# Kernel optimization log

Measured on AMD Instinct MI355X. Metric: run time of the kernel, lower is better.

The kernel has to match this reference:

```python
import jax, jax.numpy as jnp
import numpy as np

B, S, D = 4, 2048, 1024
E, H, K = 8, 2048, 2


def setup_inputs() -> dict:
    key = jax.random.key(0)
    k_x, k_g, k1, k2, k3 = jax.random.split(key, 5)
    x = jax.random.normal(k_x, (B, S, D), dtype=jnp.float32)
    # nn.Linear weight layout is [out, in]
    Wg = jax.random.normal(k_g, (E, D), dtype=jnp.float32) * 0.02   # gate
    W1 = jax.random.normal(k1, (E, H, D), dtype=jnp.float32) * 0.02  # fc1, stacked over experts
    W2 = jax.random.normal(k2, (E, H, D), dtype=jnp.float32) * 0.02  # fc2
    W3 = jax.random.normal(k3, (E, D, H), dtype=jnp.float32) * 0.02  # fc3
    return {"x": x, "Wg": Wg, "W1": W1, "W2": W2, "W3": W3}


def reference(x, Wg, W1, W2, W3):
    # gating
    scores = jnp.einsum("bsd,ed->bse", x, Wg)                 # [B,S,E]
    topk_scores, topk_idx = jax.lax.top_k(scores, K)          # [B,S,K]
    topk_probs = jax.nn.softmax(topk_scores, axis=-1)         # [B,S,K]
    # scatter top-k probs back to a dense [B,S,E] gate (indices are distinct per token)
    gating = jnp.sum(jax.nn.one_hot(topk_idx, E, dtype=x.dtype) * topk_probs[..., None], axis=-2)  # [B,S,E]
    # dense compute-all-experts SwiGLU (faithful to source)
    h1 = jnp.einsum("bsd,ehd->bseh", x, W1)                   # [B,S,E,H]
    h2 = jnp.einsum("bsd,ehd->bseh", x, W2)
    hidden = jax.nn.silu(h1) * h2
    expert_out = jnp.einsum("bseh,edh->bsed", hidden, W3)     # [B,S,E,D]
    y = jnp.einsum("bse,bsed->bsd", gating, expert_out)       # weighted combine
    return y
```

## Files before the change

kernel.cpp:

```cpp
#include <hip/hip_runtime.h>
#include <hip/hip_bf16.h>
#include <cstdint>
#include <cstddef>

typedef unsigned short u16;
typedef uint32_t u32;
typedef __attribute__((ext_vector_type(4))) float f32x4;
typedef __attribute__((ext_vector_type(8))) short bf16x8;

#define NTOK 8192
#define DIM  1024
#define HID  2048
#define NEXP 8
#define MAXT1 72
#define MAXT2 136

#define GLD16(g, l) __builtin_amdgcn_global_load_lds( \
    (const __attribute__((address_space(1))) void*)(g), \
    (__attribute__((address_space(3))) void*)(l), 16, 0, 0)

#define WAITV(n) asm volatile("s_waitcnt vmcnt(" #n ")" ::: "memory")

__device__ __forceinline__ u16 f2bf(float f) {
  __hip_bfloat16 h = __float2bfloat16(f);
  return __builtin_bit_cast(u16, h);
}
__device__ __forceinline__ float bf2f(short s) {
  u32 u = ((u32)(u16)s) << 16;
  return __builtin_bit_cast(float, u);
}

__device__ __forceinline__ const bf16x8* lds_frag(const u16* base, int row, int chunk) {
  return (const bf16x8*)(base + row * 64 + ((chunk ^ (row & 7)) << 3));
}

__global__ __launch_bounds__(256) void convert_bf16_kernel(
    const float4* __restrict__ src, ushort4* __restrict__ dst, int n4) {
  int stride = gridDim.x * blockDim.x;
  for (int i = blockIdx.x * blockDim.x + threadIdx.x; i < n4; i += stride) {
    float4 v = src[i];
    ushort4 o;
    o.x = f2bf(v.x); o.y = f2bf(v.y); o.z = f2bf(v.z); o.w = f2bf(v.w);
    dst[i] = o;
  }
}

__global__ __launch_bounds__(256) void gating_kernel(
    const float4* __restrict__ x4, const float4* __restrict__ Wg4,
    int* __restrict__ gate_idx, float* __restrict__ gate_prob,
    u16* __restrict__ Xb) {
  int tid = threadIdx.x, w = tid >> 6, l = tid & 63;
  int t = blockIdx.x * 4 + w;

  float4 xv[4];
#pragma unroll
  for (int j = 0; j < 4; ++j)
    xv[j] = x4[(size_t)t * 256 + l + 64 * j];

  float acc[NEXP];
#pragma unroll
  for (int e = 0; e < NEXP; ++e) acc[e] = 0.f;
#pragma unroll
  for (int e = 0; e < NEXP; ++e)
#pragma unroll
    for (int j = 0; j < 4; ++j) {
      float4 wv = Wg4[e * 256 + l + 64 * j];
      acc[e] += xv[j].x * wv.x + xv[j].y * wv.y + xv[j].z * wv.z + xv[j].w * wv.w;
    }

#pragma unroll
  for (int j = 0; j < 4; ++j) {
    ushort4 o;
    o.x = f2bf(xv[j].x); o.y = f2bf(xv[j].y);
    o.z = f2bf(xv[j].z); o.w = f2bf(xv[j].w);
    *(ushort4*)&Xb[(size_t)t * DIM + (l + 64 * j) * 4] = o;
  }

#pragma unroll
  for (int off = 32; off >= 1; off >>= 1)
#pragma unroll
    for (int e = 0; e < NEXP; ++e)
      acc[e] += __shfl_xor(acc[e], off);

  if (l == 0) {
    float best = -1e30f, sec = -1e30f;
    int bi = 0, si = 0;
#pragma unroll
    for (int e = 0; e < NEXP; ++e) {
      float s = acc[e];
      if (s > best)      { sec = best; si = bi; best = s; bi = e; }
      else if (s > sec)  { sec = s; si = e; }
    }
    float e1  = __expf(sec - best);
    float inv = 1.f / (1.f + e1);
    gate_idx[t * 2]      = bi;
    gate_idx[t * 2 + 1]  = si;
    gate_prob[t * 2]     = inv;
    gate_prob[t * 2 + 1] = e1 * inv;
  }
}

__global__ __launch_bounds__(256) void hist_kernel(
    const int* __restrict__ gate_idx, int* __restrict__ counts) {
  __shared__ int h[NEXP];
  int tid = threadIdx.x;
  if (tid < NEXP) h[tid] = 0;
  __syncthreads();
  int i = blockIdx.x * 256 + tid;
  atomicAdd(&h[gate_idx[i]], 1);
  __syncthreads();
  if (tid < NEXP) atomicAdd(&counts[tid], h[tid]);
}

__global__ void scan_kernel(const int* __restrict__ counts,
                            int* __restrict__ offs, int* __restrict__ cursors,
                            int* __restrict__ tileE1, int* __restrict__ tileRow1,
                            int* __restrict__ nt1,
                            int* __restrict__ tileE2, int* __restrict__ tileRow2,
                            int* __restrict__ nt2) {
  if (threadIdx.x == 0 && blockIdx.x == 0) {
    int s = 0;
    for (int e = 0; e < NEXP; ++e) { offs[e] = s; cursors[e] = s; s += counts[e]; }
    int n1 = 0, n2 = 0;
    for (int e = 0; e < NEXP; ++e) {
      for (int r = 0; r < counts[e]; r += 256) { tileE1[n1] = e; tileRow1[n1] = r; ++n1; }
      for (int r = 0; r < counts[e]; r += 128) { tileE2[n2] = e; tileRow2[n2] = r; ++n2; }
    }
    *nt1 = n1; *nt2 = n2;
  }
}

__global__ __launch_bounds__(256) void scatter_kernel(
    const int* __restrict__ gate_idx, int* __restrict__ cursors,
    int* __restrict__ list, int* __restrict__ pos_of) {
  __shared__ int lc[NEXP];
  __shared__ int lbase[NEXP];
  int tid = threadIdx.x;
  if (tid < NEXP) lc[tid] = 0;
  __syncthreads();
  int i = blockIdx.x * 256 + tid;
  int e = gate_idx[i];
  int lp = atomicAdd(&lc[e], 1);
  __syncthreads();
  if (tid < NEXP) lbase[tid] = atomicAdd(&cursors[tid], lc[tid]);
  __syncthreads();
  int pos = lbase[e] + lp;
  list[pos] = i;
  pos_of[i] = pos;
}

__global__ __launch_bounds__(512, 2) void gemm1_kernel(
    const u16* __restrict__ Xb, const u16* __restrict__ W1b,
    const u16* __restrict__ W2b, const int* __restrict__ list,
    const int* __restrict__ offs, const int* __restrict__ counts,
    const int* __restrict__ tileE, const int* __restrict__ tileRow,
    const int* __restrict__ n_tiles, u16* __restrict__ hidden) {
  int flat = blockIdx.x + MAXT1 * blockIdx.y;
  int nf = (flat & 7) * (MAXT1 * (HID / 128) / 8) + (flat >> 3);
  int bx = nf % MAXT1;
  int tn = nf / MAXT1;
  if (bx >= *n_tiles) return;
  int e = tileE[bx], row0 = tileRow[bx];
  int n_e = counts[e], off_e = offs[e];
  __shared__ u16 As[2][256 * 64];
  __shared__ u16 B1s[2][128 * 64];
  __shared__ u16 B2s[2][128 * 64];
  int tid = threadIdx.x, w = tid >> 6, l = tid & 63;
  const u16* W1e = W1b + (size_t)e * HID * DIM;
  const u16* W2e = W2b + (size_t)e * HID * DIM;

  int schunk = ((l & 7) ^ (l >> 3)) * 8;
  u32 offA[4];
#pragma unroll
  for (int j = 0; j < 4; ++j) {
    int r = w * 32 + j * 8 + (l >> 3);
    int idx = row0 + r;
    int entry = list[off_e + (idx < n_e ? idx : 0)];
    offA[j] = (u32)(entry >> 1) * DIM + schunk;
  }
  u32 offB[2];
#pragma unroll
  for (int j = 0; j < 2; ++j) {
    int r = w * 16 + j * 8 + (l >> 3);
    offB[j] = (u32)(tn * 128 + r) * DIM + schunk;
  }

#define STAGE1(buf, kt) do { u32 kof_ = (u32)(kt) * 64;                        \
    _Pragma("unroll")                                                          \
    for (int j = 0; j < 4; ++j) GLD16(Xb + offA[j] + kof_, &As[buf][w * 2048 + j * 512]); \
    _Pragma("unroll")                                                          \
    for (int j = 0; j < 2; ++j) {                                              \
      GLD16(W1e + offB[j] + kof_, &B1s[buf][w * 1024 + j * 512]);              \
      GLD16(W2e + offB[j] + kof_, &B2s[buf][w * 1024 + j * 512]);              \
    } } while (0)

  f32x4 acc1[4][4], acc2[4][4];
#pragma unroll
  for (int mi = 0; mi < 4; ++mi)
#pragma unroll
    for (int ni = 0; ni < 4; ++ni) {
      acc1[mi][ni] = (f32x4){0.f, 0.f, 0.f, 0.f};
      acc2[mi][ni] = (f32x4){0.f, 0.f, 0.f, 0.f};
    }
  int wm = w >> 1, wn = w & 1;

  STAGE1(0, 0);
  STAGE1(1, 1);
  for (int kt = 0; kt < DIM / 64; ++kt) {
    if (kt < DIM / 64 - 1) { WAITV(8); } else { WAITV(0); }
    __builtin_amdgcn_s_barrier();
    int cur = kt & 1;
    const u16* Ab  = As[cur];
    const u16* B1b = B1s[cur];
    const u16* B2b = B2s[cur];
#pragma unroll
    for (int ks = 0; ks < 2; ++ks) {
      bf16x8 a[4], b1[4], b2[4];
#pragma unroll
      for (int mi = 0; mi < 4; ++mi)
        a[mi] = *lds_frag(Ab, wm * 64 + mi * 16 + (l & 15), ks * 4 + (l >> 4));
#pragma unroll
      for (int ni = 0; ni < 4; ++ni) {
        b1[ni] = *lds_frag(B1b, wn * 64 + ni * 16 + (l & 15), ks * 4 + (l >> 4));
        b2[ni] = *lds_frag(B2b, wn * 64 + ni * 16 + (l & 15), ks * 4 + (l >> 4));
      }
#pragma unroll
      for (int mi = 0; mi < 4; ++mi)
#pragma unroll
        for (int ni = 0; ni < 4; ++ni) {
          acc1[mi][ni] = __builtin_amdgcn_mfma_f32_16x16x32_bf16(a[mi], b1[ni], acc1[mi][ni], 0, 0, 0);
          acc2[mi][ni] = __builtin_amdgcn_mfma_f32_16x16x32_bf16(a[mi], b2[ni], acc2[mi][ni], 0, 0, 0);
        }
    }
    asm volatile("" ::: "memory");
    __builtin_amdgcn_s_barrier();
    if (kt + 2 < DIM / 64) STAGE1(cur, kt + 2);
  }

#pragma unroll
  for (int mi = 0; mi < 4; ++mi) {
#pragma unroll
    for (int i = 0; i < 4; ++i) {
      int m_loc = wm * 64 + mi * 16 + (l >> 4) * 4 + i;
      int idx = row0 + m_loc;
      if (idx < n_e) {
        size_t pos = (size_t)(off_e + idx);
#pragma unroll
        for (int ni = 0; ni < 4; ++ni) {
          int h_loc = tn * 128 + wn * 64 + ni * 16 + (l & 15);
          float h1 = acc1[mi][ni][i];
          float h2 = acc2[mi][ni][i];
          float hv = h1 / (1.f + __expf(-h1)) * h2;
          hidden[pos * HID + h_loc] = f2bf(hv);
        }
      }
    }
  }
}

__global__ __launch_bounds__(256, 2) void gemm2_kernel(
    const u16* __restrict__ hidden, const u16* __restrict__ W3b,
    const int* __restrict__ offs, const int* __restrict__ counts,
    const int* __restrict__ tileE, const int* __restrict__ tileRow,
    const int* __restrict__ n_tiles, u16* __restrict__ eout) {
  int flat = blockIdx.x + MAXT2 * blockIdx.y;
  int nf = (flat & 7) * (MAXT2 * (DIM / 128) / 8) + (flat >> 3);
  int bx = nf % MAXT2;
  int tn = nf / MAXT2;
  if (bx >= *n_tiles) return;
  int e = tileE[bx], row0 = tileRow[bx];
  int n_e = counts[e], off_e = offs[e];
  __shared__ u16 As[2][128 * 64];
  __shared__ u16 Bs[2][128 * 64];
  int tid = threadIdx.x, w = tid >> 6, l = tid & 63;
  const u16* W3e = W3b + (size_t)e * DIM * HID;

  int schunk = ((l & 7) ^ (l >> 3)) * 8;
  u32 offA[4], offB[4];
#pragma unroll
  for (int j = 0; j < 4; ++j) {
    int r = w * 32 + j * 8 + (l >> 3);
    int idx = row0 + r;
    int pos = off_e + (idx < n_e ? idx : 0);
    offA[j] = (u32)pos * HID + schunk;
    offB[j] = (u32)(tn * 128 + r) * HID + schunk;
  }

#define STAGE2(buf, kt) do { u32 kof_ = (u32)(kt) * 64;                        \
    _Pragma("unroll")                                                          \
    for (int j = 0; j < 4; ++j) {                                              \
      GLD16(hidden + offA[j] + kof_, &As[buf][w * 2048 + j * 512]);            \
      GLD16(W3e    + offB[j] + kof_, &Bs[buf][w * 2048 + j * 512]);            \
    } } while (0)

  f32x4 acc[4][4];
#pragma unroll
  for (int mi = 0; mi < 4; ++mi)
#pragma unroll
    for (int ni = 0; ni < 4; ++ni) acc[mi][ni] = (f32x4){0.f, 0.f, 0.f, 0.f};
  int wm = w >> 1, wn = w & 1;

  STAGE2(0, 0);
  STAGE2(1, 1);
  for (int kt = 0; kt < HID / 64; ++kt) {
    if (kt < HID / 64 - 1) { WAITV(8); } else { WAITV(0); }
    __builtin_amdgcn_s_barrier();
    int cur = kt & 1;
    const u16* Ab = As[cur];
    const u16* Bb = Bs[cur];
#pragma unroll
    for (int ks = 0; ks < 2; ++ks) {
      bf16x8 a[4], b[4];
#pragma unroll
      for (int mi = 0; mi < 4; ++mi)
        a[mi] = *lds_frag(Ab, wm * 64 + mi * 16 + (l & 15), ks * 4 + (l >> 4));
#pragma unroll
      for (int ni = 0; ni < 4; ++ni)
        b[ni] = *lds_frag(Bb, wn * 64 + ni * 16 + (l & 15), ks * 4 + (l >> 4));
#pragma unroll
      for (int mi = 0; mi < 4; ++mi)
#pragma unroll
        for (int ni = 0; ni < 4; ++ni)
          acc[mi][ni] = __builtin_amdgcn_mfma_f32_16x16x32_bf16(a[mi], b[ni], acc[mi][ni], 0, 0, 0);
    }
    asm volatile("" ::: "memory");
    __builtin_amdgcn_s_barrier();
    if (kt + 2 < HID / 64) STAGE2(cur, kt + 2);
  }

#pragma unroll
  for (int mi = 0; mi < 4; ++mi) {
#pragma unroll
    for (int i = 0; i < 4; ++i) {
      int m_loc = wm * 64 + mi * 16 + (l >> 4) * 4 + i;
      int idx = row0 + m_loc;
      if (idx < n_e) {
        size_t pos = (size_t)(off_e + idx);
#pragma unroll
        for (int ni = 0; ni < 4; ++ni) {
          int d_loc = tn * 128 + wn * 64 + ni * 16 + (l & 15);
          eout[pos * DIM + d_loc] = f2bf(acc[mi][ni][i]);
        }
      }
    }
  }
}

__global__ __launch_bounds__(256) void combine_kernel(
    const u16* __restrict__ eout, const int* __restrict__ pos_of,
    const float* __restrict__ gate_prob, float* __restrict__ out) {
  int gid = blockIdx.x * 256 + threadIdx.x;
  int t = gid >> 7, dq = (gid & 127) * 8;
  int p0 = pos_of[t * 2], p1 = pos_of[t * 2 + 1];
  float w0 = gate_prob[t * 2], w1 = gate_prob[t * 2 + 1];
  bf16x8 e0 = *(const bf16x8*)&eout[(size_t)p0 * DIM + dq];
  bf16x8 e1 = *(const bf16x8*)&eout[(size_t)p1 * DIM + dq];
  float4 o0, o1;
  o0.x = w0 * bf2f(e0[0]) + w1 * bf2f(e1[0]);
  o0.y = w0 * bf2f(e0[1]) + w1 * bf2f(e1[1]);
  o0.z = w0 * bf2f(e0[2]) + w1 * bf2f(e1[2]);
  o0.w = w0 * bf2f(e0[3]) + w1 * bf2f(e1[3]);
  o1.x = w0 * bf2f(e0[4]) + w1 * bf2f(e1[4]);
  o1.y = w0 * bf2f(e0[5]) + w1 * bf2f(e1[5]);
  o1.z = w0 * bf2f(e0[6]) + w1 * bf2f(e1[6]);
  o1.w = w0 * bf2f(e0[7]) + w1 * bf2f(e1[7]);
  float4* op = (float4*)&out[(size_t)t * DIM + dq];
  op[0] = o0; op[1] = o1;
}

extern "C" void kernel_launch(void* const* d_in, const int* in_sizes, int n_in,
                              void* d_out, int out_size, void* d_ws, size_t ws_size,
                              hipStream_t stream) {
  const float* x  = (const float*)d_in[0];
  const float* Wg = (const float*)d_in[1];
  const float* W1 = (const float*)d_in[2];
  const float* W2 = (const float*)d_in[3];
  const float* W3 = (const float*)d_in[4];
  float* out = (float*)d_out;

  char* wsb = (char*)d_ws;
  int*   counts    = (int*)(wsb + 0);
  int*   cursors   = (int*)(wsb + 64);
  int*   offs      = (int*)(wsb + 128);
  int*   nt1       = (int*)(wsb + 192);
  int*   nt2       = (int*)(wsb + 196);
  int*   tileE1    = (int*)(wsb + 512);
  int*   tileRow1  = (int*)(wsb + 1024);
  int*   tileE2    = (int*)(wsb + 1536);
  int*   tileRow2  = (int*)(wsb + 2560);
  int*   gate_idx  = (int*)(wsb + 4096);
  float* gate_prob = (float*)(wsb + 4096 + 65536);
  int*   pos_of    = (int*)(wsb + 4096 + 2 * 65536);
  int*   list      = (int*)(wsb + 4096 + 3 * 65536);
  u16* Xb     = (u16*)(wsb + (1 << 20));
  u16* W1b    = Xb  + (size_t)NTOK * DIM;
  u16* W2b    = W1b + (size_t)NEXP * HID * DIM;
  u16* W3b    = W2b + (size_t)NEXP * HID * DIM;
  u16* hidden = W3b + (size_t)NEXP * DIM * HID;
  u16* eout   = W1b;

  hipMemsetAsync(wsb, 0, 256, stream);

  convert_bf16_kernel<<<2048, 256, 0, stream>>>((const float4*)W1, (ushort4*)W1b, NEXP * HID * DIM / 4);
  convert_bf16_kernel<<<2048, 256, 0, stream>>>((const float4*)W2, (ushort4*)W2b, NEXP * HID * DIM / 4);
  convert_bf16_kernel<<<2048, 256, 0, stream>>>((const float4*)W3, (ushort4*)W3b, NEXP * DIM * HID / 4);

  gating_kernel<<<NTOK / 4, 256, 0, stream>>>(
      (const float4*)x, (const float4*)Wg, gate_idx, gate_prob, Xb);
  hist_kernel<<<NTOK * 2 / 256, 256, 0, stream>>>(gate_idx, counts);
  scan_kernel<<<1, 64, 0, stream>>>(counts, offs, cursors,
                                    tileE1, tileRow1, nt1, tileE2, tileRow2, nt2);
  scatter_kernel<<<NTOK * 2 / 256, 256, 0, stream>>>(gate_idx, cursors, list, pos_of);

  gemm1_kernel<<<dim3(MAXT1, HID / 128), 512, 0, stream>>>(
      Xb, W1b, W2b, list, offs, counts, tileE1, tileRow1, nt1, hidden);
  gemm2_kernel<<<dim3(MAXT2, DIM / 128), 256, 0, stream>>>(
      hidden, W3b, offs, counts, tileE2, tileRow2, nt2, eout);
  combine_kernel<<<NTOK * 128 / 256, 256, 0, stream>>>(eout, pos_of, gate_prob, out);
}
```

Baseline: 376.1 us.

## Split gemm1 k-loop into four MFMA phases with interleaved staggered global loads

```diff
diff --git a/kernel.cpp b/kernel.cpp
--- a/kernel.cpp
+++ b/kernel.cpp
@@ -20,6 +20,9 @@
     (__attribute__((address_space(3))) void*)(l), 16, 0, 0)
 
 #define WAITV(n) asm volatile("s_waitcnt vmcnt(" #n ")" ::: "memory")
+#define BAR() do { asm volatile("" ::: "memory"); \
+                   __builtin_amdgcn_s_barrier();  \
+                   asm volatile("" ::: "memory"); } while (0)
 
 __device__ __forceinline__ u16 f2bf(float f) {
   __hip_bfloat16 h = __float2bfloat16(f);
@@ -185,14 +188,15 @@
     offB[j] = (u32)(tn * 128 + r) * DIM + schunk;
   }
 
-#define STAGE1(buf, kt) do { u32 kof_ = (u32)(kt) * 64;                        \
+#define STA(buf, kt) do { u32 kof_ = (u32)(kt) * 64;                           \
     _Pragma("unroll")                                                          \
-    for (int j = 0; j < 4; ++j) GLD16(Xb + offA[j] + kof_, &As[buf][w * 2048 + j * 512]); \
+    for (int j = 0; j < 4; ++j) GLD16(Xb + offA[j] + kof_, &As[buf][w * 2048 + j * 512]); } while (0)
+#define STB1(buf, kt) do { u32 kof_ = (u32)(kt) * 64;                          \
     _Pragma("unroll")                                                          \
-    for (int j = 0; j < 2; ++j) {                                              \
-      GLD16(W1e + offB[j] + kof_, &B1s[buf][w * 1024 + j * 512]);              \
-      GLD16(W2e + offB[j] + kof_, &B2s[buf][w * 1024 + j * 512]);              \
-    } } while (0)
+    for (int j = 0; j < 2; ++j) GLD16(W1e + offB[j] + kof_, &B1s[buf][w * 1024 + j * 512]); } while (0)
+#define STB2(buf, kt) do { u32 kof_ = (u32)(kt) * 64;                          \
+    _Pragma("unroll")                                                          \
+    for (int j = 0; j < 2; ++j) GLD16(W2e + offB[j] + kof_, &B2s[buf][w * 1024 + j * 512]); } while (0)
 
   f32x4 acc1[4][4], acc2[4][4];
 #pragma unroll
@@ -203,38 +207,100 @@
       acc2[mi][ni] = (f32x4){0.f, 0.f, 0.f, 0.f};
     }
   int wm = w >> 1, wn = w & 1;
-
-  STAGE1(0, 0);
-  STAGE1(1, 1);
+  int lr = l & 15, lc = l >> 4;
+
+  STA(0, 0); STB1(0, 0); STB2(0, 0);
+  STA(1, 1); STB1(1, 1);
+  WAITV(6);
+  BAR();
+
   for (int kt = 0; kt < DIM / 64; ++kt) {
-    if (kt < DIM / 64 - 1) { WAITV(8); } else { WAITV(0); }
-    __builtin_amdgcn_s_barrier();
     int cur = kt & 1;
     const u16* Ab  = As[cur];
-    const u16* B1b = B1s[cur];
-    const u16* B2b = B2s[cur];
+    const u16* B1p = B1s[cur];
+    const u16* B2p = B2s[cur];
+    bf16x8 a[2][4], bb[2][2];
+
 #pragma unroll
     for (int ks = 0; ks < 2; ++ks) {
-      bf16x8 a[4], b1[4], b2[4];
-#pragma unroll
-      for (int mi = 0; mi < 4; ++mi)
-        a[mi] = *lds_frag(Ab, wm * 64 + mi * 16 + (l & 15), ks * 4 + (l >> 4));
-#pragma unroll
-      for (int ni = 0; ni < 4; ++ni) {
-        b1[ni] = *lds_frag(B1b, wn * 64 + ni * 16 + (l & 15), ks * 4 + (l >> 4));
-        b2[ni] = *lds_frag(B2b, wn * 64 + ni * 16 + (l & 15), ks * 4 + (l >> 4));
-      }
-#pragma unroll
-      for (int mi = 0; mi < 4; ++mi)
-#pragma unroll
-        for (int ni = 0; ni < 4; ++ni) {
-          acc1[mi][ni] = __builtin_amdgcn_mfma_f32_16x16x32_bf16(a[mi], b1[ni], acc1[mi][ni], 0, 0, 0);
-          acc2[mi][ni] = __builtin_amdgcn_mfma_f32_16x16x32_bf16(a[mi], b2[ni], acc2[mi][ni], 0, 0, 0);
-        }
-    }
-    asm volatile("" ::: "memory");
-    __builtin_amdgcn_s_barrier();
-    if (kt + 2 < DIM / 64) STAGE1(cur, kt + 2);
+#pragma unroll
+      for (int mi = 0; mi < 4; ++mi)
+        a[ks][mi] = *lds_frag(Ab, wm * 64 + mi * 16 + lr, ks * 4 + lc);
+#pragma unroll
+      for (int ni = 0; ni < 2; ++ni)
+        bb[ks][ni] = *lds_frag(B1p, wn * 64 + ni * 16 + lr, ks * 4 + lc);
+    }
+    if (kt + 1 < DIM / 64) STB2(cur ^ 1, kt + 1);
+    asm volatile("s_waitcnt lgkmcnt(8)" ::: "memory");
+    BAR();
+    asm volatile("s_waitcnt lgkmcnt(0)" ::: "memory");
+    __builtin_amdgcn_s_setprio(1);
+#pragma unroll
+    for (int ks = 0; ks < 2; ++ks)
+#pragma unroll
+      for (int mi = 0; mi < 4; ++mi)
+#pragma unroll
+        for (int ni = 0; ni < 2; ++ni)
+          acc1[mi][ni] = __builtin_amdgcn_mfma_f32_16x16x32_bf16(a[ks][mi], bb[ks][ni], acc1[mi][ni], 0, 0, 0);
+    __builtin_amdgcn_s_setprio(0);
+    BAR();
+
+#pragma unroll
+    for (int ks = 0; ks < 2; ++ks)
+#pragma unroll
+      for (int ni = 0; ni < 2; ++ni)
+        bb[ks][ni] = *lds_frag(B1p, wn * 64 + (ni + 2) * 16 + lr, ks * 4 + lc);
+    if (kt + 2 < DIM / 64) STA(cur, kt + 2);
+    BAR();
+    asm volatile("s_waitcnt lgkmcnt(0)" ::: "memory");
+    __builtin_amdgcn_s_setprio(1);
+#pragma unroll
+    for (int ks = 0; ks < 2; ++ks)
+#pragma unroll
+      for (int mi = 0; mi < 4; ++mi)
+#pragma unroll
+        for (int ni = 0; ni < 2; ++ni)
+          acc1[mi][ni + 2] = __builtin_amdgcn_mfma_f32_16x16x32_bf16(a[ks][mi], bb[ks][ni], acc1[mi][ni + 2], 0, 0, 0);
+    __builtin_amdgcn_s_setprio(0);
+    BAR();
+
+#pragma unroll
+    for (int ks = 0; ks < 2; ++ks)
+#pragma unroll
+      for (int ni = 0; ni < 2; ++ni)
+        bb[ks][ni] = *lds_frag(B2p, wn * 64 + ni * 16 + lr, ks * 4 + lc);
+    if (kt + 2 < DIM / 64) STB1(cur, kt + 2);
+    BAR();
+    asm volatile("s_waitcnt lgkmcnt(0)" ::: "memory");
+    __builtin_amdgcn_s_setprio(1);
+#pragma unroll
+    for (int ks = 0; ks < 2; ++ks)
+#pragma unroll
+      for (int mi = 0; mi < 4; ++mi)
+#pragma unroll
+        for (int ni = 0; ni < 2; ++ni)
+          acc2[mi][ni] = __builtin_amdgcn_mfma_f32_16x16x32_bf16(a[ks][mi], bb[ks][ni], acc2[mi][ni], 0, 0, 0);
+    __builtin_amdgcn_s_setprio(0);
+    BAR();
+
+#pragma unroll
+    for (int ks = 0; ks < 2; ++ks)
+#pragma unroll
+      for (int ni = 0; ni < 2; ++ni)
+        bb[ks][ni] = *lds_frag(B2p, wn * 64 + (ni + 2) * 16 + lr, ks * 4 + lc);
+    if (kt + 2 < DIM / 64) { WAITV(6); } else { WAITV(0); }
+    BAR();
+    asm volatile("s_waitcnt lgkmcnt(0)" ::: "memory");
+    __builtin_amdgcn_s_setprio(1);
+#pragma unroll
+    for (int ks = 0; ks < 2; ++ks)
+#pragma unroll
+      for (int mi = 0; mi < 4; ++mi)
+#pragma unroll
+        for (int ni = 0; ni < 2; ++ni)
+          acc2[mi][ni + 2] = __builtin_amdgcn_mfma_f32_16x16x32_bf16(a[ks][mi], bb[ks][ni], acc2[mi][ni + 2], 0, 0, 0);
+    __builtin_amdgcn_s_setprio(0);
+    BAR();
   }
 
 #pragma unroll
@@ -256,6 +322,9 @@
       }
     }
   }
+#undef STA
+#undef STB1
+#undef STB2
 }
 
 __global__ __launch_bounds__(256, 2) void gemm2_kernel(
```

After: 388.7 us. +3.4%, slower.
